# Kernel optimization log

Hardware: AMD Instinct MI355X
Metric: run time of the kernel (lower is better)

The kernel has to match this reference:

```python
import jax, jax.numpy as jnp
import numpy as np

B, N, E = 8, 50000, 800000
IN_DIM, OUT_DIM = 64, 64


def setup_inputs() -> dict:
    key = jax.random.key(0)
    k_x, k_src, k_dst, k_ws, k_bs, k_wn, k_bn = jax.random.split(key, 7)
    x = jax.random.normal(k_x, (B, N, IN_DIM), dtype=jnp.float32)
    src = jax.random.randint(k_src, (E,), 0, N, dtype=jnp.int64)
    dst = jax.random.randint(k_dst, (E,), 0, N, dtype=jnp.int64)
    edge_index = jnp.stack([src, dst], axis=1)  # (E, 2)
    # nn.Linear init: U(-1/sqrt(in_dim), 1/sqrt(in_dim))
    bound = 1.0 / np.sqrt(IN_DIM)
    W_self = jax.random.uniform(k_ws, (OUT_DIM, IN_DIM), jnp.float32, -bound, bound)
    b_self = jax.random.uniform(k_bs, (OUT_DIM,), jnp.float32, -bound, bound)
    W_neigh = jax.random.uniform(k_wn, (OUT_DIM, IN_DIM), jnp.float32, -bound, bound)
    b_neigh = jax.random.uniform(k_bn, (OUT_DIM,), jnp.float32, -bound, bound)
    return {"x": x, "edge_index": edge_index, "W_self": W_self, "b_self": b_self,
            "W_neigh": W_neigh, "b_neigh": b_neigh}


def reference(x, edge_index, W_self, b_self, W_neigh, b_neigh):
    # x: (B, N, D); edge_index: (E, 2) [src, dst], shared topology across batch
    src = edge_index[:, 0]
    dst = edge_index[:, 1]
    # scatter-add neighbor aggregation, vectorized over batch
    agg = jnp.zeros_like(x).at[:, dst].add(x[:, src])  # (B, N, D)
    h_self = jnp.einsum('bnd,od->bno', x, W_self) + b_self
    h_neigh = jnp.einsum('bnd,od->bno', agg, W_neigh) + b_neigh
    return jax.nn.relu(h_self + h_neigh)
```

## Files before the change

kernel.cpp:

```cpp
#include <hip/hip_runtime.h>

#define Bn 8
#define Nn 50000
#define En 800000
#define Dd 64
#define AS 136
#define CAP 64

typedef __attribute__((ext_vector_type(8))) unsigned short ushort8;
typedef __attribute__((ext_vector_type(8))) __bf16 bf16x8;
typedef __attribute__((ext_vector_type(4))) float floatx4;

__device__ __forceinline__ unsigned short f2bf(float f) {
  unsigned int u = __builtin_bit_cast(unsigned int, f);
  u = (u + 0x7FFFu + ((u >> 16) & 1u)) >> 16;
  return (unsigned short)u;
}

__global__ __launch_bounds__(256) void k_fconv(const float* __restrict__ x,
                                               unsigned short* __restrict__ xb,
                                               const int* __restrict__ ei,
                                               int* __restrict__ deg,
                                               unsigned short* __restrict__ bucket) {
  const size_t gid = (size_t)blockIdx.x * 256 + threadIdx.x;
  const size_t i = gid * 4;
  const float4 v = *(const float4*)(x + i);
  ushort4 o;
  o.x = f2bf(v.x); o.y = f2bf(v.y); o.z = f2bf(v.z); o.w = f2bf(v.w);
  *(ushort4*)(xb + i) = o;
  if (gid < En) {
    const int d = ei[2 * gid + 1];
    const int s = ei[2 * gid + 0];
    const int p = atomicAdd(&deg[d], 1);
    if (p < CAP) bucket[(d << 6) + p] = (unsigned short)s;
  }
}

__global__ __launch_bounds__(256, 4) void k_main(
    const unsigned short* __restrict__ xb, const unsigned short* __restrict__ bucket,
    const int* __restrict__ deg, const float* __restrict__ Ws,
    const float* __restrict__ bs, const float* __restrict__ Wn,
    const float* __restrict__ bn, float* __restrict__ out) {
  __shared__ __align__(16) unsigned short Wt[64 * AS];
  __shared__ __align__(16) unsigned short A[64 * AS];
  __shared__ float bias[64];
  __shared__ int eidx[4][64];

  const int tid = threadIdx.x;
  const int b = blockIdx.x & 7;
  const int node0 = (blockIdx.x >> 3) * 64;
  const int wave = tid >> 6;
  const int lane = tid & 63;

  for (int idx = tid; idx < 64 * 128; idx += 256) {
    int o = idx >> 7, k = idx & 127;
    float v = (k < 64) ? Ws[o * 64 + k] : Wn[o * 64 + (k - 64)];
    Wt[o * AS + k] = f2bf(v);
  }
  if (tid < 64) bias[tid] = bs[tid] + bn[tid];

  const int slot = lane >> 3;
  const int li = lane & 7;
  const int ebase = lane & 56;
  const size_t xb_base = (size_t)b * Nn * Dd;

  for (int g = 0; g < 2; ++g) {
    const int nl = wave * 16 + g * 8 + slot;
    const int node = node0 + nl;
    float acc[8] = {0.f, 0.f, 0.f, 0.f, 0.f, 0.f, 0.f, 0.f};
    if (node < Nn) {
      const int cnt = min(deg[node], CAP);
      const unsigned short* bkt = bucket + (node << 6);
      int base = 0;
      for (; base + 8 <= cnt; base += 8) {
        eidx[wave][ebase + li] = bkt[base + li];
        #pragma unroll
        for (int t = 0; t < 8; ++t) {
          const int s = eidx[wave][ebase + t];
          const uint4 v = *(const uint4*)(xb + xb_base + (size_t)s * Dd + li * 8);
          const unsigned int* w = (const unsigned int*)&v;
          #pragma unroll
          for (int j = 0; j < 4; ++j) {
            acc[2 * j] += __builtin_bit_cast(float, w[j] << 16);
            acc[2 * j + 1] += __builtin_bit_cast(float, w[j] & 0xFFFF0000u);
          }
        }
      }
      const int rem = cnt - base;
      if (rem > 0) {
        if (li < rem) eidx[wave][ebase + li] = bkt[base + li];
        for (int t = 0; t < rem; ++t) {
          const int s = eidx[wave][ebase + t];
          const uint4 v = *(const uint4*)(xb + xb_base + (size_t)s * Dd + li * 8);
          const unsigned int* w = (const unsigned int*)&v;
          #pragma unroll
          for (int j = 0; j < 4; ++j) {
            acc[2 * j] += __builtin_bit_cast(float, w[j] << 16);
            acc[2 * j + 1] += __builtin_bit_cast(float, w[j] & 0xFFFF0000u);
          }
        }
      }
      const uint4 sv = *(const uint4*)(xb + xb_base + (size_t)node * Dd + li * 8);
      *(uint4*)&A[nl * AS + li * 8] = sv;
    } else {
      const uint4 z = make_uint4(0, 0, 0, 0);
      *(uint4*)&A[nl * AS + li * 8] = z;
    }
    ushort8 av;
    #pragma unroll
    for (int j = 0; j < 8; ++j) av[j] = f2bf(acc[j]);
    *(ushort8*)&A[nl * AS + 64 + li * 8] = av;
  }
  __syncthreads();

  const int col = lane & 15;
  const int quad = lane >> 4;
  bf16x8 af[4];
  {
    const unsigned short* arow = &A[(wave * 16 + col) * AS + quad * 8];
    #pragma unroll
    for (int k = 0; k < 4; ++k)
      af[k] = __builtin_bit_cast(bf16x8, *(const ushort8*)(arow + k * 32));
  }
  #pragma unroll
  for (int t = 0; t < 4; ++t) {
    floatx4 acc = {0.f, 0.f, 0.f, 0.f};
    const unsigned short* brow = &Wt[(t * 16 + col) * AS + quad * 8];
    #pragma unroll
    for (int k = 0; k < 4; ++k) {
      bf16x8 bf = __builtin_bit_cast(bf16x8, *(const ushort8*)(brow + k * 32));
      acc = __builtin_amdgcn_mfma_f32_16x16x32_bf16(af[k], bf, acc, 0, 0, 0);
    }
    const float bv = bias[t * 16 + col];
    #pragma unroll
    for (int r = 0; r < 4; ++r) {
      const int node = node0 + wave * 16 + quad * 4 + r;
      if (node < Nn) {
        float v = acc[r] + bv;
        out[((size_t)b * Nn + node) * Dd + t * 16 + col] = v > 0.f ? v : 0.f;
      }
    }
  }
}

#define OFF_XB 0ull
#define OFF_DEG 51200000ull
#define OFF_BKT 51400000ull
#define WS_NEED 57800000ull

extern "C" void kernel_launch(void* const* d_in, const int* in_sizes, int n_in,
                              void* d_out, int out_size, void* d_ws,
                              size_t ws_size, hipStream_t stream) {
  const float* x = (const float*)d_in[0];
  const int* ei = (const int*)d_in[1];
  const float* Ws = (const float*)d_in[2];
  const float* bs = (const float*)d_in[3];
  const float* Wn = (const float*)d_in[4];
  const float* bn = (const float*)d_in[5];
  float* out = (float*)d_out;

  if (ws_size < WS_NEED) return;

  char* ws = (char*)d_ws;
  unsigned short* xb = (unsigned short*)(ws + OFF_XB);
  int* deg = (int*)(ws + OFF_DEG);
  unsigned short* bucket = (unsigned short*)(ws + OFF_BKT);

  hipMemsetAsync(deg, 0, Nn * sizeof(int), stream);
  k_fconv<<<(Bn * Nn * Dd / 4) / 256, 256, 0, stream>>>(x, xb, ei, deg, bucket);
  const int ntiles = (Nn + 63) / 64;
  k_main<<<ntiles * Bn, 256, 0, stream>>>(xb, bucket, deg, Ws, bs, Wn, bn, out);
}
```

Measured before the change: 338.0 us.

## Pre-convert weights to bf16 once, drop LDS weight tile, use nontemporal accesses

Weight conversion to bf16 moves into the conversion kernel, so each main-kernel block no longer converts both weight matrices into a shared-memory tile. B fragments are loaded directly from global memory into registers, which frees LDS and may raise occupancy but increases register pressure. Other changes: nontemporal loads and stores for the bulk conversion and the output, two edges handled per thread with one 128-bit load, and 32-bit byte-offset address math for the gathers. These target per-block setup cost and cache pollution from streaming data.

Result: slower. 369.4 us (+9.3%).

```diff
diff --git a/kernel.cpp b/kernel.cpp
--- a/kernel.cpp
+++ b/kernel.cpp
@@ -10,6 +10,8 @@
 typedef __attribute__((ext_vector_type(8))) unsigned short ushort8;
 typedef __attribute__((ext_vector_type(8))) __bf16 bf16x8;
 typedef __attribute__((ext_vector_type(4))) float floatx4;
+typedef __attribute__((ext_vector_type(4))) unsigned int uint4v;
+typedef __attribute__((ext_vector_type(4))) unsigned short ushort4v;
 
 __device__ __forceinline__ unsigned short f2bf(float f) {
   unsigned int u = __builtin_bit_cast(unsigned int, f);
@@ -21,29 +23,43 @@
                                                unsigned short* __restrict__ xb,
                                                const int* __restrict__ ei,
                                                int* __restrict__ deg,
-                                               unsigned short* __restrict__ bucket) {
+                                               unsigned short* __restrict__ bucket,
+                                               const float* __restrict__ Ws,
+                                               const float* __restrict__ Wn,
+                                               unsigned short* __restrict__ Wsb,
+                                               unsigned short* __restrict__ Wnb) {
   const size_t gid = (size_t)blockIdx.x * 256 + threadIdx.x;
   const size_t i = gid * 4;
-  const float4 v = *(const float4*)(x + i);
-  ushort4 o;
+  const floatx4 v = __builtin_nontemporal_load((const floatx4*)(x + i));
+  ushort4v o;
   o.x = f2bf(v.x); o.y = f2bf(v.y); o.z = f2bf(v.z); o.w = f2bf(v.w);
-  *(ushort4*)(xb + i) = o;
-  if (gid < En) {
-    const int d = ei[2 * gid + 1];
-    const int s = ei[2 * gid + 0];
-    const int p = atomicAdd(&deg[d], 1);
-    if (p < CAP) bucket[(d << 6) + p] = (unsigned short)s;
+  __builtin_nontemporal_store(o, (ushort4v*)(xb + i));
+  if (gid < En / 2) {
+    const int4 e2 = *(const int4*)(ei + 4 * gid);
+    const int p0 = atomicAdd(&deg[e2.y], 1);
+    if (p0 < CAP) bucket[(e2.y << 6) + p0] = (unsigned short)e2.x;
+    const int p1 = atomicAdd(&deg[e2.w], 1);
+    if (p1 < CAP) bucket[(e2.w << 6) + p1] = (unsigned short)e2.z;
+  }
+  if (gid < 1024) {
+    const int j = (int)gid * 4;
+    const float4 ws = *(const float4*)(Ws + j);
+    ushort4 a;
+    a.x = f2bf(ws.x); a.y = f2bf(ws.y); a.z = f2bf(ws.z); a.w = f2bf(ws.w);
+    *(ushort4*)(Wsb + j) = a;
+    const float4 wn = *(const float4*)(Wn + j);
+    ushort4 c;
+    c.x = f2bf(wn.x); c.y = f2bf(wn.y); c.z = f2bf(wn.z); c.w = f2bf(wn.w);
+    *(ushort4*)(Wnb + j) = c;
   }
 }
 
 __global__ __launch_bounds__(256, 4) void k_main(
     const unsigned short* __restrict__ xb, const unsigned short* __restrict__ bucket,
-    const int* __restrict__ deg, const float* __restrict__ Ws,
-    const float* __restrict__ bs, const float* __restrict__ Wn,
+    const int* __restrict__ deg, const unsigned short* __restrict__ Wsb,
+    const float* __restrict__ bs, const unsigned short* __restrict__ Wnb,
     const float* __restrict__ bn, float* __restrict__ out) {
-  __shared__ __align__(16) unsigned short Wt[64 * AS];
   __shared__ __align__(16) unsigned short A[64 * AS];
-  __shared__ float bias[64];
   __shared__ int eidx[4][64];
 
   const int tid = threadIdx.x;
@@ -52,17 +68,10 @@
   const int wave = tid >> 6;
   const int lane = tid & 63;
 
-  for (int idx = tid; idx < 64 * 128; idx += 256) {
-    int o = idx >> 7, k = idx & 127;
-    float v = (k < 64) ? Ws[o * 64 + k] : Wn[o * 64 + (k - 64)];
-    Wt[o * AS + k] = f2bf(v);
-  }
-  if (tid < 64) bias[tid] = bs[tid] + bn[tid];
-
   const int slot = lane >> 3;
   const int li = lane & 7;
   const int ebase = lane & 56;
-  const size_t xb_base = (size_t)b * Nn * Dd;
+  const char* xb_b = (const char*)xb + (size_t)b * Nn * Dd * 2;
 
   for (int g = 0; g < 2; ++g) {
     const int nl = wave * 16 + g * 8 + slot;
@@ -76,13 +85,13 @@
         eidx[wave][ebase + li] = bkt[base + li];
         #pragma unroll
         for (int t = 0; t < 8; ++t) {
-          const int s = eidx[wave][ebase + t];
-          const uint4 v = *(const uint4*)(xb + xb_base + (size_t)s * Dd + li * 8);
-          const unsigned int* w = (const unsigned int*)&v;
+          const unsigned int off =
+              ((unsigned int)eidx[wave][ebase + t] << 7) | (li << 4);
+          const uint4v v = *(const uint4v*)(xb_b + off);
           #pragma unroll
           for (int j = 0; j < 4; ++j) {
-            acc[2 * j] += __builtin_bit_cast(float, w[j] << 16);
-            acc[2 * j + 1] += __builtin_bit_cast(float, w[j] & 0xFFFF0000u);
+            acc[2 * j] += __builtin_bit_cast(float, v[j] << 16);
+            acc[2 * j + 1] += __builtin_bit_cast(float, v[j] & 0xFFFF0000u);
           }
         }
       }
@@ -90,31 +99,46 @@
       if (rem > 0) {
         if (li < rem) eidx[wave][ebase + li] = bkt[base + li];
         for (int t = 0; t < rem; ++t) {
-          const int s = eidx[wave][ebase + t];
-          const uint4 v = *(const uint4*)(xb + xb_base + (size_t)s * Dd + li * 8);
-          const unsigned int* w = (const unsigned int*)&v;
+          const unsigned int off =
+              ((unsigned int)eidx[wave][ebase + t] << 7) | (li << 4);
+          const uint4v v = *(const uint4v*)(xb_b + off);
           #pragma unroll
           for (int j = 0; j < 4; ++j) {
-            acc[2 * j] += __builtin_bit_cast(float, w[j] << 16);
-            acc[2 * j + 1] += __builtin_bit_cast(float, w[j] & 0xFFFF0000u);
+            acc[2 * j] += __builtin_bit_cast(float, v[j] << 16);
+            acc[2 * j + 1] += __builtin_bit_cast(float, v[j] & 0xFFFF0000u);
           }
         }
       }
-      const uint4 sv = *(const uint4*)(xb + xb_base + (size_t)node * Dd + li * 8);
-      *(uint4*)&A[nl * AS + li * 8] = sv;
+      const uint4v sv =
+          *(const uint4v*)(xb_b + (((unsigned int)node << 7) | (li << 4)));
+      *(uint4v*)&A[nl * AS + li * 8] = sv;
     } else {
-      const uint4 z = make_uint4(0, 0, 0, 0);
-      *(uint4*)&A[nl * AS + li * 8] = z;
+      const uint4v z = {0, 0, 0, 0};
+      *(uint4v*)&A[nl * AS + li * 8] = z;
     }
     ushort8 av;
     #pragma unroll
     for (int j = 0; j < 8; ++j) av[j] = f2bf(acc[j]);
     *(ushort8*)&A[nl * AS + 64 + li * 8] = av;
   }
-  __syncthreads();
 
   const int col = lane & 15;
   const int quad = lane >> 4;
+  bf16x8 bfrag[4][4];
+  float bv[4];
+  #pragma unroll
+  for (int t = 0; t < 4; ++t) {
+    const int o = t * 16 + col;
+    bv[t] = bs[o] + bn[o];
+    #pragma unroll
+    for (int k = 0; k < 4; ++k) {
+      const unsigned short* src =
+          ((k < 2) ? Wsb : Wnb) + o * 64 + (k & 1) * 32 + quad * 8;
+      bfrag[t][k] = __builtin_bit_cast(bf16x8, *(const ushort8*)src);
+    }
+  }
+  __syncthreads();
+
   bf16x8 af[4];
   {
     const unsigned short* arow = &A[(wave * 16 + col) * AS + quad * 8];
@@ -125,19 +149,17 @@
   #pragma unroll
   for (int t = 0; t < 4; ++t) {
     floatx4 acc = {0.f, 0.f, 0.f, 0.f};
-    const unsigned short* brow = &Wt[(t * 16 + col) * AS + quad * 8];
-    #pragma unroll
-    for (int k = 0; k < 4; ++k) {
-      bf16x8 bf = __builtin_bit_cast(bf16x8, *(const ushort8*)(brow + k * 32));
-      acc = __builtin_amdgcn_mfma_f32_16x16x32_bf16(af[k], bf, acc, 0, 0, 0);
-    }
-    const float bv = bias[t * 16 + col];
+    #pragma unroll
+    for (int k = 0; k < 4; ++k)
+      acc = __builtin_amdgcn_mfma_f32_16x16x32_bf16(af[k], bfrag[t][k], acc, 0, 0, 0);
     #pragma unroll
     for (int r = 0; r < 4; ++r) {
       const int node = node0 + wave * 16 + quad * 4 + r;
       if (node < Nn) {
-        float v = acc[r] + bv;
-        out[((size_t)b * Nn + node) * Dd + t * 16 + col] = v > 0.f ? v : 0.f;
+        float v = acc[r] + bv[t];
+        __builtin_nontemporal_store(
+            v > 0.f ? v : 0.f,
+            out + ((size_t)b * Nn + node) * Dd + t * 16 + col);
       }
     }
   }
@@ -146,7 +168,9 @@
 #define OFF_XB 0ull
 #define OFF_DEG 51200000ull
 #define OFF_BKT 51400000ull
-#define WS_NEED 57800000ull
+#define OFF_WSB 57800000ull
+#define OFF_WNB 57808192ull
+#define WS_NEED 57816384ull
 
 extern "C" void kernel_launch(void* const* d_in, const int* in_sizes, int n_in,
                               void* d_out, int out_size, void* d_ws,
@@ -165,9 +189,12 @@
   unsigned short* xb = (unsigned short*)(ws + OFF_XB);
   int* deg = (int*)(ws + OFF_DEG);
   unsigned short* bucket = (unsigned short*)(ws + OFF_BKT);
-
-  hipMemsetAsync(deg, 0, Nn * sizeof(int), stream);
-  k_fconv<<<(Bn * Nn * Dd / 4) / 256, 256, 0, stream>>>(x, xb, ei, deg, bucket);
+  unsigned short* Wsb = (unsigned short*)(ws + OFF_WSB);
+  unsigned short* Wnb = (unsigned short*)(ws + OFF_WNB);
+
+  (void)hipMemsetAsync(deg, 0, Nn * sizeof(int), stream);
+  k_fconv<<<(Bn * Nn * Dd / 4) / 256, 256, 0, stream>>>(x, xb, ei, deg, bucket,
+                                                        Ws, Wn, Wsb, Wnb);
   const int ntiles = (Nn + 63) / 64;
-  k_main<<<ntiles * Bn, 256, 0, stream>>>(xb, bucket, deg, Ws, bs, Wn, bn, out);
-}
+  k_main<<<ntiles * Bn, 256, 0, stream>>>(xb, bucket, deg, Wsb, bs, Wnb, bn, out);
+}
```
